# Kernel tuning notes

Hardware: AMD Instinct MI355X
Metric: run time of the kernel (lower is better)

The kernel has to match this reference:

```python
import jax, jax.numpy as jnp
import numpy as np
from jax import lax

H = 128      # hidden_size
KK = 4       # num_kernels (TemporalConv k)
NL = 2       # rgcn num_layers
C = 32       # convtranse channels
KS = 3       # convtranse kernel_size
NE = 40000   # num_ents
NR = 256     # num_rels
T = 4        # history length
E = 100000   # edges per snapshot
NT = 1024    # num query triplets


def _norm(x):
    return x / jnp.maximum(jnp.linalg.norm(x, axis=-1, keepdims=True), 1e-12)


def _gru(x, h, wih, whh, bih, bhh):
    gi = x @ wih.T + bih
    gh = h @ whh.T + bhh
    ir, iz, inn = jnp.split(gi, 3, axis=-1)
    hr, hz, hn = jnp.split(gh, 3, axis=-1)
    r = jax.nn.sigmoid(ir + hr)
    z = jax.nn.sigmoid(iz + hz)
    n = jnp.tanh(inn + r * hn)
    return (1.0 - z) * n + z * h


def _tconv(e, t, w, b, pw, pb):
    # e: (N,H), t: (1,H) -> kernels (KK,1,H//KK)
    v = (t @ w.T + b).reshape(KK, 1, -1)
    f = lax.conv_general_dilated(e[:, None, :], v, (1,), 'VALID',
                                 dimension_numbers=('NCH', 'OIH', 'NCH'))  # (N,KK,H-H//KK+1)
    return f.reshape(f.shape[0], -1) @ pw.T + pb


def _convtranse(x, ck, cb, fw, fb):
    p = KS // 2
    y = lax.conv_general_dilated(x, ck, (1,), [(p, p)],
                                 dimension_numbers=('NCH', 'OIH', 'NCH')) + cb[None, :, None]
    y = jax.nn.relu(y)
    return jax.nn.relu(y.reshape(y.shape[0], -1) @ fw.T + fb)


def _agg_rel(nf, s, d, r):
    # dense (num_rels, num_nodes) bool mask via scatter, then per-rel mean of touched nodes
    mask = jnp.zeros((NR, NE), bool).at[r, s].set(True).at[r, d].set(True)
    m = mask.astype(nf.dtype)
    su = m @ nf
    c = m.sum(1, keepdims=True)
    return jnp.where(c > 0, su / jnp.maximum(c, 1.0), 0.0)


def _rgcn(h, ef, s, d, wn, ws, b):
    ones = jnp.ones((s.shape[0], 1), h.dtype)
    for l in range(NL):
        msg = h[s] + ef
        sums = jax.ops.segment_sum(msg, d, num_segments=NE)
        cnt = jax.ops.segment_sum(ones, d, num_segments=NE)
        agg = sums / jnp.maximum(cnt, 1.0)
        h = jax.nn.relu(agg @ wn[l] + h @ ws[l] + b[l])
    return h


def setup_inputs() -> dict:
    key = jax.random.key(0)
    ks = jax.random.split(key, 40)
    f32 = jnp.float32
    pin = H * KK - H + KK  # TemporalConv pooling in-features
    inp = {
        'ent_embeds': jax.random.normal(ks[0], (NE, H), f32),
        'rel_embeds': jax.random.normal(ks[1], (NR, H), f32) * 0.1,
        'mmt_embed': jax.random.normal(ks[2], (1, H), f32) * 0.1,
        'tc_w': jax.random.normal(ks[3], (H, H), f32) * 0.05,
        'tc_b': jnp.zeros((H,), f32),
        'tc_pw': jax.random.normal(ks[4], (H, pin), f32) * 0.05,
        'tc_pb': jnp.zeros((H,), f32),
        'gru1_wih': jax.random.normal(ks[5], (3 * H, 2 * H), f32) * 0.05,
        'gru1_whh': jax.random.normal(ks[6], (3 * H, H), f32) * 0.05,
        'gru1_bih': jnp.zeros((3 * H,), f32),
        'gru1_bhh': jnp.zeros((3 * H,), f32),
        'l1_wih': jax.random.normal(ks[7], (3 * H, H), f32) * 0.05,
        'l1_whh': jax.random.normal(ks[8], (3 * H, H), f32) * 0.05,
        'l1_bih': jnp.zeros((3 * H,), f32),
        'l1_bhh': jnp.zeros((3 * H,), f32),
        'l2_wih': jax.random.normal(ks[9], (3 * H, H), f32) * 0.05,
        'l2_whh': jax.random.normal(ks[10], (3 * H, H), f32) * 0.05,
        'l2_bih': jnp.zeros((3 * H,), f32),
        'l2_bhh': jnp.zeros((3 * H,), f32),
        'lin_w': jax.random.normal(ks[11], (H, H), f32) * 0.05,
        'lin_b': jnp.zeros((H,), f32),
        'rgcn_wn': jax.random.normal(ks[12], (NL, H, H), f32) * 0.05,
        'rgcn_ws': jax.random.normal(ks[13], (NL, H, H), f32) * 0.05,
        'rgcn_b': jnp.zeros((NL, H), f32),
        'oc_k': jax.random.normal(ks[14], (C, 2, KS), f32) * 0.1,
        'oc_kb': jnp.zeros((C,), f32),
        'oc_fw': jax.random.normal(ks[15], (H, C * H), f32) * 0.02,
        'oc_fb': jnp.zeros((H,), f32),
        'rc_k': jax.random.normal(ks[16], (C, 2, KS), f32) * 0.1,
        'rc_kb': jnp.zeros((C,), f32),
        'rc_fw': jax.random.normal(ks[17], (H, C * H), f32) * 0.02,
        'rc_fb': jnp.zeros((H,), f32),
        'src': jax.random.randint(ks[18], (T, E), 0, NE, jnp.int32),
        'dst': jax.random.randint(ks[19], (T, E), 0, NE, jnp.int32),
        'rid': jax.random.randint(ks[20], (T, E), 0, NR, jnp.int32),
        'subj': jax.random.randint(ks[21], (NT,), 0, NE, jnp.int32),
        'rel': jax.random.randint(ks[22], (NT,), 0, NR, jnp.int32),
        'obj': jax.random.randint(ks[23], (NT,), 0, NE, jnp.int32),
    }
    return inp


def reference(ent_embeds, rel_embeds, mmt_embed, tc_w, tc_b, tc_pw, tc_pb,
              gru1_wih, gru1_whh, gru1_bih, gru1_bhh,
              l1_wih, l1_whh, l1_bih, l1_bhh,
              l2_wih, l2_whh, l2_bih, l2_bhh,
              lin_w, lin_b, rgcn_wn, rgcn_ws, rgcn_b,
              oc_k, oc_kb, oc_fw, oc_fb, rc_k, rc_kb, rc_fw, rc_fb,
              src, dst, rid, subj, rel, obj):
    rel_param = rel_embeds  # the raw parameter, used inside the loop
    ent = _norm(ent_embeds)
    relh = _norm(rel_embeds)
    mmt = mmt_embed
    zero = jnp.zeros_like(mmt)
    for t in range(T):
        s, d, r = src[t], dst[t], rid[t]
        n_mmt = _gru(mmt, zero, l1_wih, l1_whh, l1_bih, l1_bhh)
        g = _gru(mmt, zero, l2_wih, l2_whh, l2_bih, l2_bhh)
        mmt = mmt + g * (n_mmt - mmt)
        ent = _tconv(ent, mmt, tc_w, tc_b, tc_pw, tc_pb)
        relh = _tconv(relh, mmt, tc_w, tc_b, tc_pw, tc_pb)
        rel_ent = _agg_rel(ent, s, d, r)
        gru_in = jnp.concatenate([rel_ent, rel_param], axis=-1)
        n_rel = _gru(gru_in, relh, gru1_wih, gru1_whh, gru1_bih, gru1_bhh)
        n_rel = _norm(n_rel)
        efeat = n_rel[r]
        nf = _rgcn(ent, efeat, s, d, rgcn_wn, rgcn_ws, rgcn_b)
        nf = _norm(nf)
        u = jax.nn.sigmoid(ent @ lin_w.T + lin_b)
        ent = ent + u * (nf - ent)
        relh = n_rel
    obj_pred = jnp.stack([ent[subj], relh[rel]], axis=1)    # (NT,2,H)
    obj_logit = _convtranse(obj_pred, oc_k, oc_kb, oc_fw, oc_fb) @ ent.T
    rel_pred = jnp.stack([ent[subj], ent[obj]], axis=1)
    rel_logit = _convtranse(rel_pred, rc_k, rc_kb, rc_fw, rc_fb) @ relh.T
    return obj_logit, rel_logit
```

## Files before the change

### kernel.cpp

```cpp
#include <hip/hip_runtime.h>
#include <cmath>


namespace {

constexpr int H   = 128;
constexpr int KK  = 4;
constexpr int C   = 32;
constexpr int NE  = 40000;
constexpr int NR  = 256;
constexpr int T   = 4;
constexpr int E   = 100000;
constexpr int NT  = 1024;
constexpr int PIN = 388;
constexpr int MW  = 1280;
constexpr int MWU = 1250;
constexpr int KSP = 16;
constexpr size_t NEH = (size_t)NE * H;

__device__ __forceinline__ float sigm(float x) { return 1.0f / (1.0f + expf(-x)); }

__global__ __launch_bounds__(256) void norm_rows(const float* __restrict__ in,
                                                 float* __restrict__ out, int n) {
  int row  = blockIdx.x * 4 + (threadIdx.x >> 6);
  int lane = threadIdx.x & 63;
  if (row >= n) return;
  const float2* ip = reinterpret_cast<const float2*>(in + (size_t)row * H);
  float2 v = ip[lane];
  float ss = v.x * v.x + v.y * v.y;
#pragma unroll
  for (int off = 32; off; off >>= 1) ss += __shfl_xor(ss, off);
  float inv = 1.0f / fmaxf(sqrtf(ss), 1e-12f);
  float2 o; o.x = v.x * inv; o.y = v.y * inv;
  reinterpret_cast<float2*>(out + (size_t)row * H)[lane] = o;
}

__global__ void copy_vec(const float* __restrict__ a, float* __restrict__ b, int n) {
  int i = blockIdx.x * blockDim.x + threadIdx.x;
  if (i < n) b[i] = a[i];
}

__global__ __launch_bounds__(256) void transpose128(const float* __restrict__ in,
                                                    float* __restrict__ out) {
  int i = blockIdx.x * 256 + threadIdx.x;
  int o = i >> 7, k = i & 127;
  out[k * H + o] = in[o * H + k];
}

__global__ __launch_bounds__(128) void mmt_step(
    const float* __restrict__ mmt_in,
    const float* __restrict__ w1, const float* __restrict__ bi1, const float* __restrict__ bh1,
    const float* __restrict__ w2, const float* __restrict__ bi2, const float* __restrict__ bh2,
    const float* __restrict__ tcw, const float* __restrict__ tcb,
    float* __restrict__ mmt_out, float* __restrict__ vout) {
  __shared__ float sm[H], sm2[H];
  int t = threadIdx.x;
  sm[t] = mmt_in[t];
  __syncthreads();
  float g1r = bi1[t], g1z = bi1[H + t], g1n = bi1[2 * H + t];
  float g2r = bi2[t], g2z = bi2[H + t], g2n = bi2[2 * H + t];
  {
    const float4* r1p = reinterpret_cast<const float4*>(w1 + (size_t)t * H);
    const float4* z1p = reinterpret_cast<const float4*>(w1 + (size_t)(H + t) * H);
    const float4* n1p = reinterpret_cast<const float4*>(w1 + (size_t)(2 * H + t) * H);
    const float4* r2p = reinterpret_cast<const float4*>(w2 + (size_t)t * H);
    const float4* z2p = reinterpret_cast<const float4*>(w2 + (size_t)(H + t) * H);
    const float4* n2p = reinterpret_cast<const float4*>(w2 + (size_t)(2 * H + t) * H);
    const float4* x4 = reinterpret_cast<const float4*>(sm);
    for (int k = 0; k < 32; k++) {
      float4 x = x4[k];
      float4 a = r1p[k], b = z1p[k], c = n1p[k], d = r2p[k], e = z2p[k], f = n2p[k];
      g1r += x.x * a.x + x.y * a.y + x.z * a.z + x.w * a.w;
      g1z += x.x * b.x + x.y * b.y + x.z * b.z + x.w * b.w;
      g1n += x.x * c.x + x.y * c.y + x.z * c.z + x.w * c.w;
      g2r += x.x * d.x + x.y * d.y + x.z * d.z + x.w * d.w;
      g2z += x.x * e.x + x.y * e.y + x.z * e.z + x.w * e.w;
      g2n += x.x * f.x + x.y * f.y + x.z * f.z + x.w * f.w;
    }
  }
  float r1 = sigm(g1r + bh1[t]), z1 = sigm(g1z + bh1[H + t]);
  float n1 = tanhf(g1n + r1 * bh1[2 * H + t]);
  float nmmt = (1.0f - z1) * n1;
  float r2 = sigm(g2r + bh2[t]), z2 = sigm(g2z + bh2[H + t]);
  float n2 = tanhf(g2n + r2 * bh2[2 * H + t]);
  float gg = (1.0f - z2) * n2;
  float m  = sm[t];
  float mo = m + gg * (nmmt - m);
  mmt_out[t] = mo;
  sm2[t] = mo;
  __syncthreads();
  float v = tcb[t];
  {
    const float4* wp = reinterpret_cast<const float4*>(tcw + (size_t)t * H);
    const float4* x4 = reinterpret_cast<const float4*>(sm2);
    for (int k = 0; k < 32; k++) {
      float4 x = x4[k], w = wp[k];
      v += x.x * w.x + x.y * w.y + x.z * w.z + x.w * w.w;
    }
  }
  vout[t] = v;
}

__global__ __launch_bounds__(128) void build_M(const float* __restrict__ v,
                                               const float* __restrict__ pw,
                                               float* __restrict__ MT) {
  int o = blockIdx.x, p = threadIdx.x;
  __shared__ float sp[PIN];
  __shared__ float sv[H];
  for (int i = p; i < PIN; i += H) sp[i] = pw[(size_t)o * PIN + i];
  sv[p] = v[p];
  __syncthreads();
  float acc = 0.0f;
  int jlo = p - 31 > 0 ? p - 31 : 0;
  int jhi = p < 96 ? p : 96;
#pragma unroll
  for (int k = 0; k < KK; k++)
    for (int j = jlo; j <= jhi; j++) acc += sp[k * 97 + j] * sv[k * 32 + (p - j)];
  MT[p * H + o] = acc;
}

__global__ __launch_bounds__(256) void gemm_bias(const float* __restrict__ X,
                                                 const float* __restrict__ WT,
                                                 const float* __restrict__ bias,
                                                 float* __restrict__ out) {
  __shared__ float sX[64 * H];
  int t = threadIdx.x;
  int base = blockIdx.x * 64;
  const float4* gx = reinterpret_cast<const float4*>(X + (size_t)base * H);
  float4* sx4 = reinterpret_cast<float4*>(sX);
#pragma unroll
  for (int i = 0; i < 8; i++) sx4[t + 256 * i] = gx[t + 256 * i];
  __syncthreads();
  int oq = (t & 31) * 4, ng = (t >> 5) * 8;
  float acc[8][4] = {};
  for (int k = 0; k < H; k += 4) {
    float4 w0 = *reinterpret_cast<const float4*>(&WT[(k + 0) * H + oq]);
    float4 w1 = *reinterpret_cast<const float4*>(&WT[(k + 1) * H + oq]);
    float4 w2 = *reinterpret_cast<const float4*>(&WT[(k + 2) * H + oq]);
    float4 w3 = *reinterpret_cast<const float4*>(&WT[(k + 3) * H + oq]);
#pragma unroll
    for (int m = 0; m < 8; m++) {
      float4 x = *reinterpret_cast<const float4*>(&sX[(ng + m) * H + k]);
      acc[m][0] += x.x * w0.x + x.y * w1.x + x.z * w2.x + x.w * w3.x;
      acc[m][1] += x.x * w0.y + x.y * w1.y + x.z * w2.y + x.w * w3.y;
      acc[m][2] += x.x * w0.z + x.y * w1.z + x.z * w2.z + x.w * w3.z;
      acc[m][3] += x.x * w0.w + x.y * w1.w + x.z * w2.w + x.w * w3.w;
    }
  }
  float4 b4 = *reinterpret_cast<const float4*>(&bias[oq]);
#pragma unroll
  for (int m = 0; m < 8; m++) {
    float4 o4 = {acc[m][0] + b4.x, acc[m][1] + b4.y, acc[m][2] + b4.z, acc[m][3] + b4.w};
    *reinterpret_cast<float4*>(&out[(size_t)(base + ng + m) * H + oq]) = o4;
  }
}

__global__ __launch_bounds__(256) void gemm_rgcn(const float* __restrict__ A,
                                                 const float* __restrict__ Hm,
                                                 const float* __restrict__ wn,
                                                 const float* __restrict__ ws,
                                                 const float* __restrict__ bias,
                                                 const int* __restrict__ deg,
                                                 float* __restrict__ out,
                                                 int donorm) {
  __shared__ float sA[32 * H];
  __shared__ float sH[32 * H];
  int t = threadIdx.x;
  int base = blockIdx.x * 32;
  const float4* ga = reinterpret_cast<const float4*>(A + (size_t)base * H);
  const float4* gh = reinterpret_cast<const float4*>(Hm + (size_t)base * H);
  float4* sa4 = reinterpret_cast<float4*>(sA);
  float4* sh4 = reinterpret_cast<float4*>(sH);
#pragma unroll
  for (int i = 0; i < 4; i++) { sa4[t + 256 * i] = ga[t + 256 * i]; sh4[t + 256 * i] = gh[t + 256 * i]; }
  __syncthreads();
  int oq = (t & 31) * 4, ng = (t >> 5) * 4;
  float accA[4][4] = {}, accS[4][4] = {};
  for (int k = 0; k < H; k += 4) {
    float4 n0 = *reinterpret_cast<const float4*>(&wn[(k + 0) * H + oq]);
    float4 n1 = *reinterpret_cast<const float4*>(&wn[(k + 1) * H + oq]);
    float4 n2 = *reinterpret_cast<const float4*>(&wn[(k + 2) * H + oq]);
    float4 n3 = *reinterpret_cast<const float4*>(&wn[(k + 3) * H + oq]);
    float4 s0 = *reinterpret_cast<const float4*>(&ws[(k + 0) * H + oq]);
    float4 s1 = *reinterpret_cast<const float4*>(&ws[(k + 1) * H + oq]);
    float4 s2 = *reinterpret_cast<const float4*>(&ws[(k + 2) * H + oq]);
    float4 s3 = *reinterpret_cast<const float4*>(&ws[(k + 3) * H + oq]);
#pragma unroll
    for (int m = 0; m < 4; m++) {
      float4 a = *reinterpret_cast<const float4*>(&sA[(ng + m) * H + k]);
      float4 h = *reinterpret_cast<const float4*>(&sH[(ng + m) * H + k]);
      accA[m][0] += a.x * n0.x + a.y * n1.x + a.z * n2.x + a.w * n3.x;
      accA[m][1] += a.x * n0.y + a.y * n1.y + a.z * n2.y + a.w * n3.y;
      accA[m][2] += a.x * n0.z + a.y * n1.z + a.z * n2.z + a.w * n3.z;
      accA[m][3] += a.x * n0.w + a.y * n1.w + a.z * n2.w + a.w * n3.w;
      accS[m][0] += h.x * s0.x + h.y * s1.x + h.z * s2.x + h.w * s3.x;
      accS[m][1] += h.x * s0.y + h.y * s1.y + h.z * s2.y + h.w * s3.y;
      accS[m][2] += h.x * s0.z + h.y * s1.z + h.z * s2.z + h.w * s3.z;
      accS[m][3] += h.x * s0.w + h.y * s1.w + h.z * s2.w + h.w * s3.w;
    }
  }
  float4 b4 = *reinterpret_cast<const float4*>(&bias[oq]);
  float v[4][4];
#pragma unroll
  for (int m = 0; m < 4; m++) {
    float inv = 1.0f / fmaxf((float)deg[base + ng + m], 1.0f);
    v[m][0] = fmaxf(accA[m][0] * inv + accS[m][0] + b4.x, 0.0f);
    v[m][1] = fmaxf(accA[m][1] * inv + accS[m][1] + b4.y, 0.0f);
    v[m][2] = fmaxf(accA[m][2] * inv + accS[m][2] + b4.z, 0.0f);
    v[m][3] = fmaxf(accA[m][3] * inv + accS[m][3] + b4.w, 0.0f);
  }
  if (donorm) {
#pragma unroll
    for (int m = 0; m < 4; m++) {
      float ss = v[m][0]*v[m][0] + v[m][1]*v[m][1] + v[m][2]*v[m][2] + v[m][3]*v[m][3];
#pragma unroll
      for (int off = 16; off; off >>= 1) ss += __shfl_xor(ss, off);
      float inv = 1.0f / fmaxf(sqrtf(ss), 1e-12f);
      v[m][0] *= inv; v[m][1] *= inv; v[m][2] *= inv; v[m][3] *= inv;
    }
  }
#pragma unroll
  for (int m = 0; m < 4; m++) {
    float4 o4 = {v[m][0], v[m][1], v[m][2], v[m][3]};
    *reinterpret_cast<float4*>(&out[(size_t)(base + ng + m) * H + oq]) = o4;
  }
}

__global__ __launch_bounds__(256) void gemm_update(const float* __restrict__ Xe,
                                                   const float* __restrict__ WT,
                                                   const float* __restrict__ bias,
                                                   const float* __restrict__ nf,
                                                   float* __restrict__ out) {
  __shared__ float sX[64 * H];
  int t = threadIdx.x;
  int base = blockIdx.x * 64;
  const float4* gx = reinterpret_cast<const float4*>(Xe + (size_t)base * H);
  float4* sx4 = reinterpret_cast<float4*>(sX);
#pragma unroll
  for (int i = 0; i < 8; i++) sx4[t + 256 * i] = gx[t + 256 * i];
  __syncthreads();
  int oq = (t & 31) * 4, ng = (t >> 5) * 8;
  float acc[8][4] = {};
  for (int k = 0; k < H; k += 4) {
    float4 w0 = *reinterpret_cast<const float4*>(&WT[(k + 0) * H + oq]);
    float4 w1 = *reinterpret_cast<const float4*>(&WT[(k + 1) * H + oq]);
    float4 w2 = *reinterpret_cast<const float4*>(&WT[(k + 2) * H + oq]);
    float4 w3 = *reinterpret_cast<const float4*>(&WT[(k + 3) * H + oq]);
#pragma unroll
    for (int m = 0; m < 8; m++) {
      float4 x = *reinterpret_cast<const float4*>(&sX[(ng + m) * H + k]);
      acc[m][0] += x.x * w0.x + x.y * w1.x + x.z * w2.x + x.w * w3.x;
      acc[m][1] += x.x * w0.y + x.y * w1.y + x.z * w2.y + x.w * w3.y;
      acc[m][2] += x.x * w0.z + x.y * w1.z + x.z * w2.z + x.w * w3.z;
      acc[m][3] += x.x * w0.w + x.y * w1.w + x.z * w2.w + x.w * w3.w;
    }
  }
  float4 b4 = *reinterpret_cast<const float4*>(&bias[oq]);
#pragma unroll
  for (int m = 0; m < 8; m++) {
    size_t row = (size_t)(base + ng + m) * H;
    float4 e4 = *reinterpret_cast<const float4*>(&sX[(ng + m) * H + oq]);
    float4 f4 = *reinterpret_cast<const float4*>(&nf[row + oq]);
    float4 o4 = {e4.x + sigm(acc[m][0] + b4.x) * (f4.x - e4.x),
                 e4.y + sigm(acc[m][1] + b4.y) * (f4.y - e4.y),
                 e4.z + sigm(acc[m][2] + b4.z) * (f4.z - e4.z),
                 e4.w + sigm(acc[m][3] + b4.w) * (f4.w - e4.w)};
    *reinterpret_cast<float4*>(&out[row + oq]) = o4;
  }
}

__global__ __launch_bounds__(256) void edge_prep(const int* __restrict__ s,
                                                 const int* __restrict__ d,
                                                 const int* __restrict__ r,
                                                 unsigned int* __restrict__ mask,
                                                 int* __restrict__ deg) {
  int e = blockIdx.x * 256 + threadIdx.x;
  if (e >= E) return;
  int ri = r[e], si = s[e], di = d[e];
  atomicOr(&mask[(size_t)ri * MW + (si >> 5)], 1u << (si & 31));
  atomicOr(&mask[(size_t)ri * MW + (di >> 5)], 1u << (di & 31));
  atomicAdd(&deg[di], 1);
}

__global__ __launch_bounds__(1024) void scan_deg(const int* __restrict__ deg,
                                                 int* __restrict__ rowptr,
                                                 int* __restrict__ wpos) {
  __shared__ int wsum[16];
  __shared__ int carry_s;
  int tid = threadIdx.x, lane = tid & 63, w = tid >> 6;
  if (tid == 0) carry_s = 0;
  __syncthreads();
  for (int base = 0; base < NE; base += 1024) {
    int idx = base + tid;
    int v = idx < NE ? deg[idx] : 0;
    int x = v;
#pragma unroll
    for (int off = 1; off < 64; off <<= 1) {
      int y = __shfl_up(x, off, 64);
      if (lane >= off) x += y;
    }
    if (lane == 63) wsum[w] = x;
    __syncthreads();
    int carry = carry_s;
    int wpre = 0;
    for (int i = 0; i < w; i++) wpre += wsum[i];
    int excl = carry + wpre + x - v;
    if (idx < NE) { rowptr[idx] = excl; wpos[idx] = excl; }
    __syncthreads();
    if (tid == 1023) carry_s = carry + wpre + x;
  }
  __syncthreads();
  if (tid == 0) rowptr[NE] = carry_s;
}

__global__ __launch_bounds__(256) void edge_fill(const int* __restrict__ d,
                                                 int* __restrict__ wpos,
                                                 int* __restrict__ elist) {
  int e = blockIdx.x * 256 + threadIdx.x;
  if (e >= E) return;
  int p = atomicAdd(&wpos[d[e]], 1);
  elist[p] = e;
}

__global__ __launch_bounds__(256) void rgcn_gather(const float* __restrict__ h,
                                                   const float* __restrict__ ef,
                                                   const int* __restrict__ rowptr,
                                                   const int* __restrict__ elist,
                                                   const int* __restrict__ s,
                                                   const int* __restrict__ r,
                                                   float* __restrict__ agg) {
  int node = blockIdx.x * 2 + (threadIdx.x >> 7);
  int dim  = threadIdx.x & 127;
  int b = rowptr[node], e2 = rowptr[node + 1];
  float acc = 0.0f;
  for (int i = b; i < e2; i++) {
    int e = elist[i];
    acc += h[(size_t)s[e] * H + dim] + ef[(size_t)r[e] * H + dim];
  }
  agg[(size_t)node * H + dim] = acc;
}

__global__ __launch_bounds__(128) void agg_rel_sum(const unsigned int* __restrict__ mask,
                                                   const float* __restrict__ ent,
                                                   float* __restrict__ rsum,
                                                   float* __restrict__ rcnt) {
  int rel = blockIdx.x, part = blockIdx.y, tid = threadIdx.x;
  const int WPS = (MWU + 31) / 32;
  int w0 = part * WPS;
  int w1 = w0 + WPS < MWU ? w0 + WPS : MWU;
  float acc = 0.0f, cnt = 0.0f;
  const unsigned int* mrow = mask + (size_t)rel * MW;
  for (int w = w0; w < w1; w++) {
    unsigned int bits = mrow[w];
    if (!bits) continue;
    cnt += (float)__popc(bits);
    int base = w << 5;
    while (bits) {
      int b = __ffs(bits) - 1;
      bits &= bits - 1;
      acc += ent[(size_t)(base + b) * H + tid];
    }
  }
  if (acc != 0.0f) atomicAdd(&rsum[rel * H + tid], acc);
  if (tid == 0 && cnt != 0.0f) atomicAdd(&rcnt[rel], cnt);
}

__global__ __launch_bounds__(128) void rel_gru(const float* __restrict__ rsum,
                                               const float* __restrict__ rcnt,
                                               const float* __restrict__ rel_param,
                                               const float* __restrict__ relh,
                                               const float* __restrict__ wih,
                                               const float* __restrict__ whh,
                                               const float* __restrict__ bih,
                                               const float* __restrict__ bhh,
                                               float* __restrict__ outp) {
  int rel = blockIdx.x, tid = threadIdx.x;
  __shared__ float sx[2 * H], sh[H], red[H];
  float c = rcnt[rel];
  sx[tid]     = c > 0.0f ? rsum[rel * H + tid] / fmaxf(c, 1.0f) : 0.0f;
  sx[H + tid] = rel_param[rel * H + tid];
  sh[tid]     = relh[rel * H + tid];
  __syncthreads();
  float gr = bih[tid], gz = bih[H + tid], gn = bih[2 * H + tid];
  {
    const float4* rp = reinterpret_cast<const float4*>(wih + (size_t)tid * 2 * H);
    const float4* zp = reinterpret_cast<const float4*>(wih + (size_t)(H + tid) * 2 * H);
    const float4* np = reinterpret_cast<const float4*>(wih + (size_t)(2 * H + tid) * 2 * H);
    const float4* x4 = reinterpret_cast<const float4*>(sx);
    for (int k = 0; k < 64; k++) {
      float4 x = x4[k];
      float4 a = rp[k], b = zp[k], cc = np[k];
      gr += x.x * a.x + x.y * a.y + x.z * a.z + x.w * a.w;
      gz += x.x * b.x + x.y * b.y + x.z * b.z + x.w * b.w;
      gn += x.x * cc.x + x.y * cc.y + x.z * cc.z + x.w * cc.w;
    }
  }
  float hr = bhh[tid], hz = bhh[H + tid], hn = bhh[2 * H + tid];
  {
    const float4* rp = reinterpret_cast<const float4*>(whh + (size_t)tid * H);
    const float4* zp = reinterpret_cast<const float4*>(whh + (size_t)(H + tid) * H);
    const float4* np = reinterpret_cast<const float4*>(whh + (size_t)(2 * H + tid) * H);
    const float4* h4 = reinterpret_cast<const float4*>(sh);
    for (int k = 0; k < 32; k++) {
      float4 x = h4[k];
      float4 a = rp[k], b = zp[k], cc = np[k];
      hr += x.x * a.x + x.y * a.y + x.z * a.z + x.w * a.w;
      hz += x.x * b.x + x.y * b.y + x.z * b.z + x.w * b.w;
      hn += x.x * cc.x + x.y * cc.y + x.z * cc.z + x.w * cc.w;
    }
  }
  float r = sigm(gr + hr), z = sigm(gz + hz), nn = tanhf(gn + r * hn);
  float val = (1.0f - z) * nn + z * sh[tid];
  red[tid] = val * val;
  __syncthreads();
  for (int s2 = 64; s2 > 0; s2 >>= 1) {
    if (tid < s2) red[tid] += red[tid + s2];
    __syncthreads();
  }
  float inv = 1.0f / fmaxf(sqrtf(red[0]), 1e-12f);
  outp[rel * H + tid] = val * inv;
}

__global__ __launch_bounds__(256, 8) void conv_front(const float* __restrict__ fa,
                                                     const int* __restrict__ ia,
                                                     const float* __restrict__ fbm,
                                                     const int* __restrict__ ib,
                                                     const float* __restrict__ ck,
                                                     const float* __restrict__ ckb,
                                                     const float* __restrict__ fw,
                                                     float* __restrict__ Zp) {
  __shared__ float sx[8 * 2 * H];
  __shared__ float sy[8 * 256];
  __shared__ float sck[12];
  __shared__ float sckb[2];
  int tid = threadIdx.x;
  int q0 = blockIdx.x * 8, ks = blockIdx.y;
  if (tid < 12) sck[tid] = ck[ks * 12 + tid];
  if (tid < 2)  sckb[tid] = ckb[ks * 2 + tid];
#pragma unroll
  for (int i = tid; i < 2048; i += 256) {
    int q = i >> 8, half = (i >> 7) & 1, p = i & 127;
    int node = (half ? ib : ia)[q0 + q];
    const float* srcp = (half ? fbm : fa) + (size_t)node * H + p;
    sx[i] = *srcp;
  }
  __syncthreads();
#pragma unroll
  for (int i = tid; i < 2048; i += 256) {
    int q = i >> 8, c = (i >> 7) & 1, p = i & 127;
    const float* xq = &sx[q * 256];
    float acc = sckb[c];
#pragma unroll
    for (int kk = 0; kk < 3; kk++) {
      int pos = p + kk - 1;
      if (pos >= 0 && pos < H)
        acc += xq[pos] * sck[c * 6 + kk] + xq[128 + pos] * sck[c * 6 + 3 + kk];
    }
    sy[i] = fmaxf(acc, 0.0f);
  }
  __syncthreads();
  int ot = tid & 63, qg = tid >> 6;
  const float* w0p = fw + (size_t)ot * 4096 + ks * 256;
  const float* w1p = fw + (size_t)(ot + 64) * 4096 + ks * 256;
  const float* y0p = &sy[(qg * 2 + 0) * 256];
  const float* y1p = &sy[(qg * 2 + 1) * 256];
  float a00 = 0, a01 = 0, a10 = 0, a11 = 0;
  for (int j = 0; j < 256; j += 4) {
    float4 w0 = *reinterpret_cast<const float4*>(w0p + j);
    float4 w1 = *reinterpret_cast<const float4*>(w1p + j);
    float4 y0 = *reinterpret_cast<const float4*>(y0p + j);
    float4 y1 = *reinterpret_cast<const float4*>(y1p + j);
    a00 += y0.x * w0.x + y0.y * w0.y + y0.z * w0.z + y0.w * w0.w;
    a10 += y0.x * w1.x + y0.y * w1.y + y0.z * w1.z + y0.w * w1.w;
    a01 += y1.x * w0.x + y1.y * w0.y + y1.z * w0.z + y1.w * w0.w;
    a11 += y1.x * w1.x + y1.y * w1.y + y1.z * w1.z + y1.w * w1.w;
  }
  float* zb = Zp + (size_t)ks * NT * H;
  zb[(size_t)(q0 + qg * 2 + 0) * H + ot]      = a00;
  zb[(size_t)(q0 + qg * 2 + 0) * H + ot + 64] = a10;
  zb[(size_t)(q0 + qg * 2 + 1) * H + ot]      = a01;
  zb[(size_t)(q0 + qg * 2 + 1) * H + ot + 64] = a11;
}

__global__ __launch_bounds__(256) void conv_finalize(const float* __restrict__ Zp,
                                                     const float* __restrict__ fb,
                                                     float* __restrict__ Z) {
  int i = blockIdx.x * 256 + threadIdx.x;
  int o = i & 127;
  float v = fb[o];
#pragma unroll
  for (int s = 0; s < KSP; s++) v += Zp[(size_t)s * NT * H + i];
  Z[i] = fmaxf(v, 0.0f);
}

__global__ __launch_bounds__(256) void logits_gemm2(const float* __restrict__ Z,
                                                    const float* __restrict__ F,
                                                    float* __restrict__ out,
                                                    int M) {
  __shared__ float sZ[32 * H];
  __shared__ float sF[32 * H];
  int t = threadIdx.x;
  int bq = blockIdx.y * 128, bm = blockIdx.x * 128;
  int tx = t & 15, ty = t >> 4;
  float acc[8][8] = {};
  int qld = t & 127, kh = (t >> 7) * 16;
  int mld = bm + qld;
  if (mld >= M) mld = M - 1;
  for (int kc = 0; kc < H; kc += 32) {
    __syncthreads();
    const float* zr = Z + (size_t)(bq + qld) * H + kc + kh;
    const float* fr = F + (size_t)mld * H + kc + kh;
#pragma unroll
    for (int j = 0; j < 16; j += 4) {
      float4 v = *reinterpret_cast<const float4*>(zr + j);
      sZ[(kh + j + 0) * H + qld] = v.x;
      sZ[(kh + j + 1) * H + qld] = v.y;
      sZ[(kh + j + 2) * H + qld] = v.z;
      sZ[(kh + j + 3) * H + qld] = v.w;
      float4 f = *reinterpret_cast<const float4*>(fr + j);
      sF[(kh + j + 0) * H + qld] = f.x;
      sF[(kh + j + 1) * H + qld] = f.y;
      sF[(kh + j + 2) * H + qld] = f.z;
      sF[(kh + j + 3) * H + qld] = f.w;
    }
    __syncthreads();
    for (int k = 0; k < 32; k++) {
      float4 za = *reinterpret_cast<const float4*>(&sZ[k * H + ty * 8]);
      float4 zb = *reinterpret_cast<const float4*>(&sZ[k * H + ty * 8 + 4]);
      float4 fa = *reinterpret_cast<const float4*>(&sF[k * H + tx * 8]);
      float4 fbv = *reinterpret_cast<const float4*>(&sF[k * H + tx * 8 + 4]);
      float zq[8] = {za.x, za.y, za.z, za.w, zb.x, zb.y, zb.z, zb.w};
      float fm[8] = {fa.x, fa.y, fa.z, fa.w, fbv.x, fbv.y, fbv.z, fbv.w};
#pragma unroll
      for (int i = 0; i < 8; i++)
#pragma unroll
        for (int j = 0; j < 8; j++) acc[i][j] += zq[i] * fm[j];
    }
  }
  int m0 = bm + tx * 8;
  if (m0 >= M) return;
#pragma unroll
  for (int i = 0; i < 8; i++) {
    size_t row = (size_t)(bq + ty * 8 + i) * (size_t)M + m0;
    float4 o1 = {acc[i][0], acc[i][1], acc[i][2], acc[i][3]};
    float4 o2 = {acc[i][4], acc[i][5], acc[i][6], acc[i][7]};
    *reinterpret_cast<float4*>(&out[row]) = o1;
    *reinterpret_cast<float4*>(&out[row + 4]) = o2;
  }
}

}

extern "C" void kernel_launch(void* const* d_in, const int* in_sizes, int n_in,
                              void* d_out, int out_size, void* d_ws, size_t ws_size,
                              hipStream_t stream) {
  (void)in_sizes; (void)n_in; (void)out_size; (void)ws_size;
  const float* ent_embeds = (const float*)d_in[0];
  const float* rel_embeds = (const float*)d_in[1];
  const float* mmt_embed  = (const float*)d_in[2];
  const float* tc_w  = (const float*)d_in[3];
  const float* tc_b  = (const float*)d_in[4];
  const float* tc_pw = (const float*)d_in[5];
  const float* tc_pb = (const float*)d_in[6];
  const float* g1_wih = (const float*)d_in[7];
  const float* g1_whh = (const float*)d_in[8];
  const float* g1_bih = (const float*)d_in[9];
  const float* g1_bhh = (const float*)d_in[10];
  const float* l1_wih = (const float*)d_in[11];
  const float* l1_bih = (const float*)d_in[13];
  const float* l1_bhh = (const float*)d_in[14];
  const float* l2_wih = (const float*)d_in[15];
  const float* l2_bih = (const float*)d_in[17];
  const float* l2_bhh = (const float*)d_in[18];
  const float* lin_w = (const float*)d_in[19];
  const float* lin_b = (const float*)d_in[20];
  const float* rgcn_wn = (const float*)d_in[21];
  const float* rgcn_ws = (const float*)d_in[22];
  const float* rgcn_b  = (const float*)d_in[23];
  const float* oc_k  = (const float*)d_in[24];
  const float* oc_kb = (const float*)d_in[25];
  const float* oc_fw = (const float*)d_in[26];
  const float* oc_fb = (const float*)d_in[27];
  const float* rc_k  = (const float*)d_in[28];
  const float* rc_kb = (const float*)d_in[29];
  const float* rc_fw = (const float*)d_in[30];
  const float* rc_fb = (const float*)d_in[31];
  const int* src  = (const int*)d_in[32];
  const int* dst  = (const int*)d_in[33];
  const int* rid  = (const int*)d_in[34];
  const int* qsub = (const int*)d_in[35];
  const int* qrel = (const int*)d_in[36];
  const int* qobj = (const int*)d_in[37];

  float* out = (float*)d_out;
  float* ws  = (float*)d_ws;

  size_t off = 0;
  float* entF = ws + off; off += NEH;
  float* relhB[3] = {ws + off, ws + off + (size_t)NR * H, ws + off + 2 * (size_t)NR * H};
  off += 3 * (size_t)NR * H;
  float* rel_sum = ws + off; off += (size_t)NR * H;
  float* rcnt    = ws + off; off += NR;
  float* mmtbuf0 = ws + off; off += H;
  float* mmtbuf1 = ws + off; off += H;
  float* vbuf    = ws + off; off += H;
  float* MT      = ws + off; off += (size_t)H * H;
  float* WTlin   = ws + off; off += (size_t)H * H;
  float* Zo      = ws + off; off += (size_t)NT * H;
  float* Zr      = ws + off; off += (size_t)NT * H;
  unsigned int* mask = (unsigned int*)(ws + off); off += (size_t)NR * MW;

  float* B[4] = {out, out + NEH, out + 2 * NEH, out + 3 * NEH};
  int* itail   = (int*)(out + 4 * NEH);
  int* deg     = itail;
  int* rowptr  = itail + NE;
  int* wpos    = itail + 2 * NE + 1;
  int* elist   = itail + 3 * NE + 1;
  float* mmtb[2] = {mmtbuf0, mmtbuf1};
  float* Zp16 = out;

  norm_rows<<<(NE + 3) / 4, 256, 0, stream>>>(ent_embeds, B[0], NE);
  norm_rows<<<(NR + 3) / 4, 256, 0, stream>>>(rel_embeds, relhB[0], NR);
  copy_vec<<<1, 128, 0, stream>>>(mmt_embed, mmtbuf0, H);
  transpose128<<<64, 256, 0, stream>>>(lin_w, WTlin);

  int cur = 0, curRelh = 0;
  for (int t = 0; t < T; t++) {
    int fr[3], fi = 0;
    for (int b = 0; b < 4; b++) if (b != cur) fr[fi++] = b;
    int bX = fr[0], bG = fr[1], bY = fr[2];
    const int* s_t = src + (size_t)t * E;
    const int* d_t = dst + (size_t)t * E;
    const int* r_t = rid + (size_t)t * E;

    mmt_step<<<1, 128, 0, stream>>>(mmtb[t & 1], l1_wih, l1_bih, l1_bhh,
                                    l2_wih, l2_bih, l2_bhh, tc_w, tc_b,
                                    mmtb[(t + 1) & 1], vbuf);
    build_M<<<H, H, 0, stream>>>(vbuf, tc_pw, MT);
    gemm_bias<<<NE / 64, 256, 0, stream>>>(B[cur], MT, tc_pb, B[bX]);
    gemm_bias<<<NR / 64, 256, 0, stream>>>(relhB[curRelh], MT, tc_pb, relhB[2]);

    hipMemsetAsync(mask, 0, (size_t)NR * MW * 4, stream);
    hipMemsetAsync(deg, 0, (size_t)NE * 4, stream);
    edge_prep<<<(E + 255) / 256, 256, 0, stream>>>(s_t, d_t, r_t, mask, deg);

    hipMemsetAsync(rel_sum, 0, ((size_t)NR * H + NR) * 4, stream);
    agg_rel_sum<<<dim3(NR, 32), 128, 0, stream>>>(mask, B[bX], rel_sum, rcnt);
    int nextRelh = 1 - curRelh;
    rel_gru<<<NR, 128, 0, stream>>>(rel_sum, rcnt, rel_embeds, relhB[2],
                                    g1_wih, g1_whh, g1_bih, g1_bhh, relhB[nextRelh]);

    scan_deg<<<1, 1024, 0, stream>>>(deg, rowptr, wpos);
    edge_fill<<<(E + 255) / 256, 256, 0, stream>>>(d_t, wpos, elist);

    rgcn_gather<<<NE / 2, 256, 0, stream>>>(B[bX], relhB[nextRelh], rowptr, elist, s_t, r_t, B[bG]);
    gemm_rgcn<<<NE / 32, 256, 0, stream>>>(B[bG], B[bX], rgcn_wn, rgcn_ws, rgcn_b, deg, B[bY], 0);
    rgcn_gather<<<NE / 2, 256, 0, stream>>>(B[bY], relhB[nextRelh], rowptr, elist, s_t, r_t, B[bG]);
    gemm_rgcn<<<NE / 32, 256, 0, stream>>>(B[bG], B[bY], rgcn_wn + H * H, rgcn_ws + H * H,
                                           rgcn_b + H, deg, B[cur], 1);

    float* entDst = (t == T - 1) ? entF : B[bY];
    gemm_update<<<NE / 64, 256, 0, stream>>>(B[bX], WTlin, lin_b, B[cur], entDst);

    cur = bY;
    curRelh = nextRelh;
  }

  float* relhF = relhB[curRelh];

  conv_front<<<dim3(NT / 8, KSP), 256, 0, stream>>>(entF, qsub, relhF, qrel, oc_k, oc_kb, oc_fw, Zp16);
  conv_finalize<<<NT * H / 256, 256, 0, stream>>>(Zp16, oc_fb, Zo);
  conv_front<<<dim3(NT / 8, KSP), 256, 0, stream>>>(entF, qsub, entF, qobj, rc_k, rc_kb, rc_fw, Zp16);
  conv_finalize<<<NT * H / 256, 256, 0, stream>>>(Zp16, rc_fb, Zr);

  logits_gemm2<<<dim3((NE + 127) / 128, NT / 128), 256, 0, stream>>>(Zo, entF, out, NE);
  logits_gemm2<<<dim3(NR / 128, NT / 128), 256, 0, stream>>>(Zr, relhF, out + (size_t)NT * NE, NR);
}
```

Baseline: 2.310 ms.

## Split ConvTransE into conv-relu pass and register-tiled split-K GEMM with transposed weights

Replaces the fused conv_front kernel, which recomputed the gather and conv per K-split and did a 2x2 per-thread dot product, with two kernels. The first materialises the full ReLU conv output Y (NT x 4096) once. The second runs a 4x4 register-tiled split-K GEMM against a pre-transposed FC weight, with 32 K-splits. This is meant to cut redundant conv and gather work and improve weight reuse and coalescing, at the cost of extra global traffic for Y, two transpose launches per call, and twice as many partials for conv_finalize to reduce.

```diff
diff --git a/kernel.cpp b/kernel.cpp
--- a/kernel.cpp
+++ b/kernel.cpp
@@ -15,7 +15,8 @@
 constexpr int PIN = 388;
 constexpr int MW  = 1280;
 constexpr int MWU = 1250;
-constexpr int KSP = 16;
+constexpr int KC  = 4096;
+constexpr int KSP = 32;
 constexpr size_t NEH = (size_t)NE * H;
 
 __device__ __forceinline__ float sigm(float x) { return 1.0f / (1.0f + expf(-x)); }
@@ -45,6 +46,13 @@
   int i = blockIdx.x * 256 + threadIdx.x;
   int o = i >> 7, k = i & 127;
   out[k * H + o] = in[o * H + k];
+}
+
+__global__ __launch_bounds__(256) void transposeFW(const float* __restrict__ in,
+                                                   float* __restrict__ out) {
+  int i = blockIdx.x * 256 + threadIdx.x;
+  int o = i >> 12, k = i & 4095;
+  out[(size_t)k * 128 + o] = in[i];
 }
 
 __global__ __launch_bounds__(128) void mmt_step(
@@ -421,65 +429,77 @@
   outp[rel * H + tid] = val * inv;
 }
 
-__global__ __launch_bounds__(256, 8) void conv_front(const float* __restrict__ fa,
-                                                     const int* __restrict__ ia,
-                                                     const float* __restrict__ fbm,
-                                                     const int* __restrict__ ib,
-                                                     const float* __restrict__ ck,
-                                                     const float* __restrict__ ckb,
-                                                     const float* __restrict__ fw,
-                                                     float* __restrict__ Zp) {
+__global__ __launch_bounds__(256) void conv_relu(const float* __restrict__ fa,
+                                                 const int* __restrict__ ia,
+                                                 const float* __restrict__ fbm,
+                                                 const int* __restrict__ ib,
+                                                 const float* __restrict__ ck,
+                                                 const float* __restrict__ ckb,
+                                                 float* __restrict__ Y) {
   __shared__ float sx[8 * 2 * H];
-  __shared__ float sy[8 * 256];
-  __shared__ float sck[12];
-  __shared__ float sckb[2];
-  int tid = threadIdx.x;
-  int q0 = blockIdx.x * 8, ks = blockIdx.y;
-  if (tid < 12) sck[tid] = ck[ks * 12 + tid];
-  if (tid < 2)  sckb[tid] = ckb[ks * 2 + tid];
+  __shared__ float sck[C * 6];
+  __shared__ float sckb[C];
+  int tid = threadIdx.x, q0 = blockIdx.x * 8;
+  if (tid < C * 6) sck[tid] = ck[tid];
+  if (tid < C)     sckb[tid] = ckb[tid];
 #pragma unroll
   for (int i = tid; i < 2048; i += 256) {
     int q = i >> 8, half = (i >> 7) & 1, p = i & 127;
     int node = (half ? ib : ia)[q0 + q];
-    const float* srcp = (half ? fbm : fa) + (size_t)node * H + p;
-    sx[i] = *srcp;
-  }
-  __syncthreads();
-#pragma unroll
-  for (int i = tid; i < 2048; i += 256) {
-    int q = i >> 8, c = (i >> 7) & 1, p = i & 127;
-    const float* xq = &sx[q * 256];
-    float acc = sckb[c];
-#pragma unroll
-    for (int kk = 0; kk < 3; kk++) {
-      int pos = p + kk - 1;
-      if (pos >= 0 && pos < H)
-        acc += xq[pos] * sck[c * 6 + kk] + xq[128 + pos] * sck[c * 6 + 3 + kk];
-    }
-    sy[i] = fmaxf(acc, 0.0f);
-  }
-  __syncthreads();
-  int ot = tid & 63, qg = tid >> 6;
-  const float* w0p = fw + (size_t)ot * 4096 + ks * 256;
-  const float* w1p = fw + (size_t)(ot + 64) * 4096 + ks * 256;
-  const float* y0p = &sy[(qg * 2 + 0) * 256];
-  const float* y1p = &sy[(qg * 2 + 1) * 256];
-  float a00 = 0, a01 = 0, a10 = 0, a11 = 0;
-  for (int j = 0; j < 256; j += 4) {
-    float4 w0 = *reinterpret_cast<const float4*>(w0p + j);
-    float4 w1 = *reinterpret_cast<const float4*>(w1p + j);
-    float4 y0 = *reinterpret_cast<const float4*>(y0p + j);
-    float4 y1 = *reinterpret_cast<const float4*>(y1p + j);
-    a00 += y0.x * w0.x + y0.y * w0.y + y0.z * w0.z + y0.w * w0.w;
-    a10 += y0.x * w1.x + y0.y * w1.y + y0.z * w1.z + y0.w * w1.w;
-    a01 += y1.x * w0.x + y1.y * w0.y + y1.z * w0.z + y1.w * w0.w;
-    a11 += y1.x * w1.x + y1.y * w1.y + y1.z * w1.z + y1.w * w1.w;
+    sx[i] = (half ? fbm : fa)[(size_t)node * H + p];
+  }
+  __syncthreads();
+  for (int i4 = tid; i4 < 8192; i4 += 256) {
+    int q = i4 >> 10, rr = i4 & 1023;
+    int c = rr >> 5, p0 = (rr & 31) << 2;
+    const float* x0 = &sx[q * 256];
+    const float* x1 = x0 + 128;
+    float k00 = sck[c * 6 + 0], k01 = sck[c * 6 + 1], k02 = sck[c * 6 + 2];
+    float k10 = sck[c * 6 + 3], k11 = sck[c * 6 + 4], k12 = sck[c * 6 + 5];
+    float bb = sckb[c];
+    float4 o;
+    float* op = &o.x;
+#pragma unroll
+    for (int dd = 0; dd < 4; dd++) {
+      int p = p0 + dd;
+      float acc = bb + x0[p] * k01 + x1[p] * k11;
+      if (p - 1 >= 0)  acc += x0[p - 1] * k00 + x1[p - 1] * k10;
+      if (p + 1 < H)   acc += x0[p + 1] * k02 + x1[p + 1] * k12;
+      op[dd] = fmaxf(acc, 0.0f);
+    }
+    *reinterpret_cast<float4*>(&Y[(size_t)(q0 + q) * KC + rr * 4]) = o;
+  }
+}
+
+__global__ __launch_bounds__(256) void conv_gemm(const float* __restrict__ Y,
+                                                 const float* __restrict__ fwT,
+                                                 float* __restrict__ Zp) {
+  int t = threadIdx.x;
+  int mb = blockIdx.x * 32, ks = blockIdx.y;
+  int oq = (t & 31) * 4, ng = (t >> 5) * 4;
+  const float* yb = Y + (size_t)(mb + ng) * KC + ks * 128;
+  const float* wb = fwT + (size_t)ks * 128 * H + oq;
+  float acc[4][4] = {};
+  for (int k = 0; k < 128; k += 4) {
+    float4 w0 = *reinterpret_cast<const float4*>(wb + (size_t)(k + 0) * H);
+    float4 w1 = *reinterpret_cast<const float4*>(wb + (size_t)(k + 1) * H);
+    float4 w2 = *reinterpret_cast<const float4*>(wb + (size_t)(k + 2) * H);
+    float4 w3 = *reinterpret_cast<const float4*>(wb + (size_t)(k + 3) * H);
+#pragma unroll
+    for (int m = 0; m < 4; m++) {
+      float4 y = *reinterpret_cast<const float4*>(yb + (size_t)m * KC + k);
+      acc[m][0] += y.x * w0.x + y.y * w1.x + y.z * w2.x + y.w * w3.x;
+      acc[m][1] += y.x * w0.y + y.y * w1.y + y.z * w2.y + y.w * w3.y;
+      acc[m][2] += y.x * w0.z + y.y * w1.z + y.z * w2.z + y.w * w3.z;
+      acc[m][3] += y.x * w0.w + y.y * w1.w + y.z * w2.w + y.w * w3.w;
+    }
   }
   float* zb = Zp + (size_t)ks * NT * H;
-  zb[(size_t)(q0 + qg * 2 + 0) * H + ot]      = a00;
-  zb[(size_t)(q0 + qg * 2 + 0) * H + ot + 64] = a10;
-  zb[(size_t)(q0 + qg * 2 + 1) * H + ot]      = a01;
-  zb[(size_t)(q0 + qg * 2 + 1) * H + ot + 64] = a11;
+#pragma unroll
+  for (int m = 0; m < 4; m++) {
+    float4 o4 = {acc[m][0], acc[m][1], acc[m][2], acc[m][3]};
+    *reinterpret_cast<float4*>(&zb[(size_t)(mb + ng + m) * H + oq]) = o4;
+  }
 }
 
 __global__ __launch_bounds__(256) void conv_finalize(const float* __restrict__ Zp,
@@ -617,7 +637,10 @@
   int* wpos    = itail + 2 * NE + 1;
   int* elist   = itail + 3 * NE + 1;
   float* mmtb[2] = {mmtbuf0, mmtbuf1};
-  float* Zp16 = out;
+  float* Ybuf  = out;
+  float* Zp    = out + (size_t)NT * KC;
+  float* fwTo  = Zp + (size_t)KSP * NT * H;
+  float* fwTr  = fwTo + (size_t)KC * H;
 
   norm_rows<<<(NE + 3) / 4, 256, 0, stream>>>(ent_embeds, B[0], NE);
   norm_rows<<<(NR + 3) / 4, 256, 0, stream>>>(rel_embeds, relhB[0], NR);
@@ -668,10 +691,16 @@
 
   float* relhF = relhB[curRelh];
 
-  conv_front<<<dim3(NT / 8, KSP), 256, 0, stream>>>(entF, qsub, relhF, qrel, oc_k, oc_kb, oc_fw, Zp16);
-  conv_finalize<<<NT * H / 256, 256, 0, stream>>>(Zp16, oc_fb, Zo);
-  conv_front<<<dim3(NT / 8, KSP), 256, 0, stream>>>(entF, qsub, entF, qobj, rc_k, rc_kb, rc_fw, Zp16);
-  conv_finalize<<<NT * H / 256, 256, 0, stream>>>(Zp16, rc_fb, Zr);
+  transposeFW<<<2048, 256, 0, stream>>>(oc_fw, fwTo);
+  transposeFW<<<2048, 256, 0, stream>>>(rc_fw, fwTr);
+
+  conv_relu<<<NT / 8, 256, 0, stream>>>(entF, qsub, relhF, qrel, oc_k, oc_kb, Ybuf);
+  conv_gemm<<<dim3(NT / 32, KSP), 256, 0, stream>>>(Ybuf, fwTo, Zp);
+  conv_finalize<<<NT * H / 256, 256, 0, stream>>>(Zp, oc_fb, Zo);
+
+  conv_relu<<<NT / 8, 256, 0, stream>>>(entF, qsub, entF, qobj, rc_k, rc_kb, Ybuf);
+  conv_gemm<<<dim3(NT / 32, KSP), 256, 0, stream>>>(Ybuf, fwTr, Zp);
+  conv_finalize<<<NT * H / 256, 256, 0, stream>>>(Zp, rc_fb, Zr);
 
   logits_gemm2<<<dim3((NE + 127) / 128, NT / 128), 256, 0, stream>>>(Zo, entF, out, NE);
   logits_gemm2<<<dim3(NR / 128, NT / 128), 256, 0, stream>>>(Zr, relhF, out + (size_t)NT * NE, NR);
```

Result: faster. 2.215 ms (-4.1%).
